# Kernel optimization log

Measured on AMD Instinct MI355X. Metric: run time of the kernel, lower is better.

## Reference

```python
import jax, jax.numpy as jnp
import numpy as np

EPS = 1e-12  # torch F.normalize eps

def _l2norm(v):
    return v / jnp.maximum(jnp.linalg.norm(v, axis=-1, keepdims=True), EPS)

def setup_inputs() -> dict:
    key = jax.random.key(0)
    x = jax.random.normal(key, (64, 64, 10, 512), dtype=jnp.float32)
    w = jnp.asarray(10.0, dtype=jnp.float32)
    b = jnp.asarray(-5.0, dtype=jnp.float32)
    return {"x": x, "w": w, "b": b}

def reference(x, w, b):
    B, N, M, D = x.shape
    NM = N * M
    x_flat = _l2norm(x.reshape(B, NM, D))                      # [B, NM, D]
    c_full = _l2norm(jnp.mean(x, axis=2))                      # [B, N, D]
    # leave-one-out centroid: (M * normalized_full_centroid - x) / (M - 1), then normalize
    c_excl = _l2norm(((M * c_full[:, :, None, :] - x) / (M - 1)).reshape(B, NM, D))  # [B, NM, D]
    # cosine sim of each utterance vs every (normalized) full centroid
    sim = jnp.einsum("bkd,bnd->bkn", x_flat, c_full)           # [B, NM, N]
    # replace own-speaker column with leave-one-out similarity (avoids [B,NM,N,D] blowup)
    excl_sim = jnp.sum(x_flat * c_excl, axis=-1)               # [B, NM]
    speaker_ids = jnp.repeat(jnp.arange(N), M)                 # [NM]
    rows = jnp.arange(NM)
    sim = sim.at[:, rows, speaker_ids].set(excl_sim)
    logits = w * sim + b                                       # [B, NM, N]
    logp = jax.nn.log_softmax(logits, axis=-1)
    # cross-entropy with targets = speaker_ids per row, mean over B*NM
    nll = -logp[:, rows, speaker_ids]                          # [B, NM]
    return jnp.mean(nll)
```

## Files before the change

kernel.cpp:

```cpp
#include <hip/hip_runtime.h>
#include <math.h>

static constexpr int Bn = 64;
static constexpr int Nn = 64;
static constexpr int Mn = 10;
static constexpr int Dn = 512;
static constexpr int NMn = Nn * Mn;
static constexpr int RT = 32;
static constexpr int NBLK2 = Bn * (NMn / RT);
static constexpr float EPSV = 1e-12f;

typedef unsigned short u16;
typedef unsigned int u32;
typedef __attribute__((ext_vector_type(8))) __bf16 bf16x8;
typedef __attribute__((ext_vector_type(4))) float f32x4;

static __device__ __forceinline__ u16 f2bf(float f) {
  u32 u = __float_as_uint(f);
  u = u + 0x7fffu + ((u >> 16) & 1u);
  return (u16)(u >> 16);
}


__global__ __launch_bounds__(256) void centroid_k(const float* __restrict__ x,
                                                  u16* __restrict__ ch2,
                                                  float* __restrict__ out) {
  const int bn = blockIdx.x;
  const int tid = threadIdx.x;
  const int f4 = tid & 127;
  const int mg = tid >> 7;
  const int wv = tid >> 6, ln = tid & 63;
  const float4* xp = (const float4*)(x + (size_t)bn * (Mn * Dn));

  if (bn == 0 && tid == 0) out[0] = 0.f;

  float4 a = {0.f, 0.f, 0.f, 0.f};
#pragma unroll
  for (int k = 0; k < 5; ++k) {
    const float4 v = xp[(2 * k + mg) * 128 + f4];
    a.x += v.x; a.y += v.y; a.z += v.z; a.w += v.w;
  }
  __shared__ float4 cred[128];
  if (mg == 1) cred[f4] = a;
  __syncthreads();

  float4 c = {0.f, 0.f, 0.f, 0.f};
  float cs = 0.f;
  if (mg == 0) {
    c = cred[f4];
    c.x += a.x; c.y += a.y; c.z += a.z; c.w += a.w;
    cs = c.x * c.x + c.y * c.y + c.z * c.z + c.w * c.w;
  }
#pragma unroll
  for (int t = 1; t < 64; t <<= 1) cs += __shfl_xor(cs, t, 64);
  __shared__ float csred[2];
  if (mg == 0 && ln == 0) csred[wv] = cs;
  __syncthreads();
  if (mg == 0) {
    const float scale = 1.0f / fmaxf(sqrtf(csred[0] + csred[1]), EPSV);
    const u16 h0 = f2bf(c.x * scale), h1 = f2bf(c.y * scale);
    const u16 h2 = f2bf(c.z * scale), h3 = f2bf(c.w * scale);
    uint2 w;
    w.x = (u32)h0 | ((u32)h1 << 16);
    w.y = (u32)h2 | ((u32)h3 << 16);
    const int n = bn & (Nn - 1), bb = bn >> 6;
    const size_t off = (((size_t)bb * 16 + (f4 >> 3)) * Nn + n) * 32 + ((f4 & 7) * 4);
    *(uint2*)(ch2 + off) = w;
  }
}

__global__ __launch_bounds__(512) void gemm_loss_k(const float* __restrict__ x,
                                                   const u16* __restrict__ ch2,
                                                   const float* __restrict__ wp,
                                                   const float* __restrict__ bp,
                                                   float* __restrict__ out) {
  __shared__ float S[8][16][65];
  __shared__ float SQ[2][4][16];
  __shared__ float nred[8];

  const int b = blockIdx.x / (NMn / RT);
  const int rt = blockIdx.x % (NMn / RT);
  const int row0 = rt * RT;
  const int tid = threadIdx.x, wv = tid >> 6, ln = tid & 63;
  const int lr = ln & 15;
  const int lkb = (ln >> 4) * 8;
  const int rh = wv >> 2;
  const int q = wv & 3;
  const int k0 = q * 128;

  const float* arow = x + ((size_t)b * NMn + row0 + rh * 16 + lr) * Dn + k0 + lkb;
  const u16* brow = ch2 + (((size_t)b * 16 + q * 4) * Nn) * 32 + (size_t)lr * 32 + lkb;

  f32x4 acc0 = {0.f, 0.f, 0.f, 0.f};
  f32x4 acc1 = acc0, acc2 = acc0, acc3 = acc0;
  float sq = 0.f;

#pragma unroll
  for (int kk = 0; kk < 128; kk += 32) {
    const u16* bp8 = brow + (size_t)(kk >> 5) * (Nn * 32);
    const float4 f0 = *(const float4*)(arow + kk);
    const float4 f1 = *(const float4*)(arow + kk + 4);
    const bf16x8 b0 = *(const bf16x8*)(bp8);
    const bf16x8 b1 = *(const bf16x8*)(bp8 + 16 * 32);
    const bf16x8 b2 = *(const bf16x8*)(bp8 + 32 * 32);
    const bf16x8 b3 = *(const bf16x8*)(bp8 + 48 * 32);
    const float v[8] = {f0.x, f0.y, f0.z, f0.w, f1.x, f1.y, f1.z, f1.w};
    bf16x8 ah;
#pragma unroll
    for (int i = 0; i < 8; ++i) {
      ah[i] = (__bf16)v[i];
      sq = fmaf(v[i], v[i], sq);
    }
    acc0 = __builtin_amdgcn_mfma_f32_16x16x32_bf16(ah, b0, acc0, 0, 0, 0);
    acc1 = __builtin_amdgcn_mfma_f32_16x16x32_bf16(ah, b1, acc1, 0, 0, 0);
    acc2 = __builtin_amdgcn_mfma_f32_16x16x32_bf16(ah, b2, acc2, 0, 0, 0);
    acc3 = __builtin_amdgcn_mfma_f32_16x16x32_bf16(ah, b3, acc3, 0, 0, 0);
  }

  sq += __shfl_xor(sq, 16, 64);
  sq += __shfl_xor(sq, 32, 64);
  if (ln < 16) SQ[rh][q][lr] = sq;

  const int orow = (ln >> 4) * 4;
#pragma unroll
  for (int r = 0; r < 4; ++r) {
    S[wv][orow + r][lr] = acc0[r];
    S[wv][orow + r][16 + lr] = acc1[r];
    S[wv][orow + r][32 + lr] = acc2[r];
    S[wv][orow + r][48 + lr] = acc3[r];
  }
  __syncthreads();

  const float W = *wp, Bb = *bp;
  float lane_nll = 0.f;
#pragma unroll
  for (int i = 0; i < 4; ++i) {
    const int R = wv * 4 + i;
    const int rhh = R >> 4, rl = R & 15;
    const int krow = row0 + R;
    const int spk = krow / Mn;
    const float rn = S[rhh * 4 + 0][rl][ln] + S[rhh * 4 + 1][rl][ln] +
                     S[rhh * 4 + 2][rl][ln] + S[rhh * 4 + 3][rl][ln];
    const float x2 = SQ[rhh][0][rl] + SQ[rhh][1][rl] + SQ[rhh][2][rl] + SQ[rhh][3][rl];
    const float xn = sqrtf(x2);
    const float inv_xn = 1.0f / fmaxf(xn, EPSV);
    float sv = rn * inv_xn;
    if (ln == spk) {
      const float num = (float)Mn * rn - x2;
      const float en = sqrtf(fmaxf((float)(Mn * Mn) - 2.0f * (float)Mn * rn + x2, 0.f));
      sv = num / fmaxf(xn * en, EPSV);
    }
    const float logit = W * sv + Bb;
    float e = expf(logit);
#pragma unroll
    for (int t = 1; t < 64; t <<= 1) e += __shfl_xor(e, t, 64);
    if (ln == 0) lane_nll += logf(e);
    if (ln == spk) lane_nll -= logit;
  }
#pragma unroll
  for (int t = 1; t < 64; t <<= 1) lane_nll += __shfl_xor(lane_nll, t, 64);
  if (ln == 0) nred[wv] = lane_nll;
  __syncthreads();
  if (tid == 0) {
    float s = 0.f;
#pragma unroll
    for (int i = 0; i < 8; ++i) s += nred[i];
    atomicAdd(out, s * (1.0f / (float)(Bn * NMn)));
  }
}

static constexpr int ROWS = 8;
static constexpr int DCHUNK = 128;
static constexpr int CPAD = DCHUNK + 1;

__global__ __launch_bounds__(256) void centroid_fb_k(const float* __restrict__ x,
                                                     float* __restrict__ c) {
  const int bn = blockIdx.x;
  const float* xp = x + (size_t)bn * Mn * Dn;
  const int tid = threadIdx.x;
  float a0 = 0.f, a1 = 0.f;
#pragma unroll
  for (int m = 0; m < Mn; ++m) {
    a0 += xp[m * Dn + tid];
    a1 += xp[m * Dn + tid + 256];
  }
  float s = a0 * a0 + a1 * a1;
#pragma unroll
  for (int m = 1; m < 64; m <<= 1) s += __shfl_xor(s, m, 64);
  __shared__ float red[4];
  const int wv = tid >> 6, ln = tid & 63;
  if (ln == 0) red[wv] = s;
  __syncthreads();
  const float tot = red[0] + red[1] + red[2] + red[3];
  const float scale = 1.0f / fmaxf(sqrtf(tot), EPSV);
  float* cp = c + (size_t)bn * Dn;
  cp[tid] = a0 * scale;
  cp[tid + 256] = a1 * scale;
}

__global__ __launch_bounds__(256) void loss_fb_k(const float* __restrict__ x,
                                                 const float* __restrict__ c,
                                                 const float* __restrict__ wp,
                                                 const float* __restrict__ bp,
                                                 float* __restrict__ out) {
  __shared__ __align__(16) float x_lds[ROWS * Dn];
  __shared__ float c_lds[Nn * CPAD];
  __shared__ float xn2s[ROWS];
  __shared__ float sim_lds[ROWS][Nn];

  const int tid = threadIdx.x;
  const int b = blockIdx.x / (NMn / ROWS);
  const int rblk = blockIdx.x % (NMn / ROWS);
  const int row0 = rblk * ROWS;
  const float* xrow = x + ((size_t)b * NMn + row0) * Dn;
  {
    const float4* xs = (const float4*)xrow;
    float4* xd = (float4*)x_lds;
#pragma unroll
    for (int i = tid; i < ROWS * Dn / 4; i += 256) xd[i] = xs[i];
  }
  __syncthreads();
  const int wv = tid >> 6, ln = tid & 63;
  for (int r = wv; r < ROWS; r += 4) {
    float s = 0.f;
#pragma unroll
    for (int j = ln; j < Dn; j += 64) {
      const float v = x_lds[r * Dn + j];
      s += v * v;
    }
#pragma unroll
    for (int m = 1; m < 64; m <<= 1) s += __shfl_xor(s, m, 64);
    if (ln == 0) xn2s[r] = s;
  }
  const int n = tid & 63;
  const int rg = tid >> 6;
  const int r0 = rg * 2, r1 = rg * 2 + 1;
  float s0 = 0.f, s1 = 0.f;
  const float* cb_base = c + (size_t)b * Nn * Dn;
  for (int cb = 0; cb < Dn; cb += DCHUNK) {
    __syncthreads();
    for (int i = tid; i < Nn * DCHUNK; i += 256) {
      const int nn = i / DCHUNK;
      const int j = i & (DCHUNK - 1);
      c_lds[nn * CPAD + j] = cb_base[(size_t)nn * Dn + cb + j];
    }
    __syncthreads();
#pragma unroll 16
    for (int j = 0; j < DCHUNK; ++j) {
      const float cv = c_lds[n * CPAD + j];
      s0 = fmaf(x_lds[r0 * Dn + cb + j], cv, s0);
      s1 = fmaf(x_lds[r1 * Dn + cb + j], cv, s1);
    }
  }
  sim_lds[r0][n] = s0;
  sim_lds[r1][n] = s1;
  __syncthreads();
  const float W = *wp, Bb = *bp;
  float acc_nll = 0.f;
  for (int r = wv; r < ROWS; r += 4) {
    const int k = row0 + r;
    const int spk = k / Mn;
    const float rn = sim_lds[r][ln];
    const float x2 = xn2s[r];
    const float xn = sqrtf(x2);
    const float inv_xn = 1.0f / fmaxf(xn, EPSV);
    const float rspk = sim_lds[r][spk];
    float sv = rn * inv_xn;
    if (ln == spk) {
      const float num = (float)Mn * rspk - x2;
      const float en = sqrtf(fmaxf((float)(Mn * Mn) - 2.0f * (float)Mn * rspk + x2, 0.f));
      sv = num / fmaxf(xn * en, EPSV);
    }
    const float logit = W * sv + Bb;
    const float lspk = __shfl(logit, spk, 64);
    float mx = logit;
#pragma unroll
    for (int m = 1; m < 64; m <<= 1) mx = fmaxf(mx, __shfl_xor(mx, m, 64));
    float se = expf(logit - mx);
#pragma unroll
    for (int m = 1; m < 64; m <<= 1) se += __shfl_xor(se, m, 64);
    acc_nll += (mx + logf(se)) - lspk;
  }
  __shared__ float nred[4];
  if (ln == 0) nred[wv] = acc_nll;
  __syncthreads();
  if (tid == 0)
    atomicAdd(out, (nred[0] + nred[1] + nred[2] + nred[3]) * (1.0f / (float)(Bn * NMn)));
}

extern "C" void kernel_launch(void* const* d_in, const int* in_sizes, int n_in,
                              void* d_out, int out_size, void* d_ws, size_t ws_size,
                              hipStream_t stream) {
  const float* x = (const float*)d_in[0];
  const float* w = (const float*)d_in[1];
  const float* b = (const float*)d_in[2];
  float* out = (float*)d_out;

  const size_t CSZ = (size_t)Bn * 16 * Nn * 32 * sizeof(u16);
  const size_t NEED = CSZ;

  if (ws_size >= NEED) {
    u16* ch2 = (u16*)d_ws;
    hipLaunchKernelGGL(centroid_k, dim3(Bn * Nn), dim3(256), 0, stream, x, ch2, out);
    hipLaunchKernelGGL(gemm_loss_k, dim3(NBLK2), dim3(512), 0, stream,
                       x, ch2, w, b, out);
  } else {
    float* c = (float*)d_ws;
    hipMemsetAsync(out, 0, sizeof(float), stream);
    hipLaunchKernelGGL(centroid_fb_k, dim3(Bn * Nn), dim3(256), 0, stream, x, c);
    hipLaunchKernelGGL(loss_fb_k, dim3(Bn * (NMn / ROWS)), dim3(256), 0, stream,
                       x, c, w, b, out);
  }
}
```

Baseline: 46.06 us.

## Process two speakers per centroid block and swizzle gemm block order across XCDs

The centroid kernel now handles two speakers per workgroup, which halves the grid and doubles the loads in flight per thread. The loss kernel remaps block IDs so that consecutive blocks on each of the 8 XCDs cover contiguous tiles of the same batch, aiming for better L2 locality of x and the centroid tiles. The trade-offs are higher register use and fewer blocks in the centroid kernel, and the swizzle assumes NBLK2 divides evenly by 8.

```diff
diff --git a/kernel.cpp b/kernel.cpp
--- a/kernel.cpp
+++ b/kernel.cpp
@@ -25,47 +25,63 @@
 __global__ __launch_bounds__(256) void centroid_k(const float* __restrict__ x,
                                                   u16* __restrict__ ch2,
                                                   float* __restrict__ out) {
-  const int bn = blockIdx.x;
+  const int base = blockIdx.x * 2;
   const int tid = threadIdx.x;
   const int f4 = tid & 127;
   const int mg = tid >> 7;
   const int wv = tid >> 6, ln = tid & 63;
-  const float4* xp = (const float4*)(x + (size_t)bn * (Mn * Dn));
-
-  if (bn == 0 && tid == 0) out[0] = 0.f;
-
-  float4 a = {0.f, 0.f, 0.f, 0.f};
+
+  if (blockIdx.x == 0 && tid == 0) out[0] = 0.f;
+
+  const float4* xp0 = (const float4*)(x + (size_t)base * (Mn * Dn));
+  const float4* xp1 = (const float4*)(x + (size_t)(base + 1) * (Mn * Dn));
+
+  float4 a0 = {0.f, 0.f, 0.f, 0.f}, a1 = {0.f, 0.f, 0.f, 0.f};
 #pragma unroll
   for (int k = 0; k < 5; ++k) {
-    const float4 v = xp[(2 * k + mg) * 128 + f4];
-    a.x += v.x; a.y += v.y; a.z += v.z; a.w += v.w;
-  }
-  __shared__ float4 cred[128];
-  if (mg == 1) cred[f4] = a;
-  __syncthreads();
-
-  float4 c = {0.f, 0.f, 0.f, 0.f};
-  float cs = 0.f;
+    const float4 v0 = xp0[(2 * k + mg) * 128 + f4];
+    const float4 v1 = xp1[(2 * k + mg) * 128 + f4];
+    a0.x += v0.x; a0.y += v0.y; a0.z += v0.z; a0.w += v0.w;
+    a1.x += v1.x; a1.y += v1.y; a1.z += v1.z; a1.w += v1.w;
+  }
+  __shared__ float4 cred[2][128];
+  if (mg == 1) { cred[0][f4] = a0; cred[1][f4] = a1; }
+  __syncthreads();
+
+  float cs0 = 0.f, cs1 = 0.f;
+  float4 c0 = {0.f, 0.f, 0.f, 0.f}, c1 = {0.f, 0.f, 0.f, 0.f};
   if (mg == 0) {
-    c = cred[f4];
-    c.x += a.x; c.y += a.y; c.z += a.z; c.w += a.w;
-    cs = c.x * c.x + c.y * c.y + c.z * c.z + c.w * c.w;
-  }
-#pragma unroll
-  for (int t = 1; t < 64; t <<= 1) cs += __shfl_xor(cs, t, 64);
-  __shared__ float csred[2];
-  if (mg == 0 && ln == 0) csred[wv] = cs;
+    const float4 v0 = cred[0][f4];
+    c0.x = a0.x + v0.x; c0.y = a0.y + v0.y; c0.z = a0.z + v0.z; c0.w = a0.w + v0.w;
+    cs0 = c0.x * c0.x + c0.y * c0.y + c0.z * c0.z + c0.w * c0.w;
+    const float4 v1 = cred[1][f4];
+    c1.x = a1.x + v1.x; c1.y = a1.y + v1.y; c1.z = a1.z + v1.z; c1.w = a1.w + v1.w;
+    cs1 = c1.x * c1.x + c1.y * c1.y + c1.z * c1.z + c1.w * c1.w;
+  }
+#pragma unroll
+  for (int t = 1; t < 64; t <<= 1) {
+    cs0 += __shfl_xor(cs0, t, 64);
+    cs1 += __shfl_xor(cs1, t, 64);
+  }
+  __shared__ float csred[2][2];
+  if (mg == 0 && ln == 0) { csred[0][wv] = cs0; csred[1][wv] = cs1; }
   __syncthreads();
   if (mg == 0) {
-    const float scale = 1.0f / fmaxf(sqrtf(csred[0] + csred[1]), EPSV);
-    const u16 h0 = f2bf(c.x * scale), h1 = f2bf(c.y * scale);
-    const u16 h2 = f2bf(c.z * scale), h3 = f2bf(c.w * scale);
-    uint2 w;
-    w.x = (u32)h0 | ((u32)h1 << 16);
-    w.y = (u32)h2 | ((u32)h3 << 16);
-    const int n = bn & (Nn - 1), bb = bn >> 6;
-    const size_t off = (((size_t)bb * 16 + (f4 >> 3)) * Nn + n) * 32 + ((f4 & 7) * 4);
-    *(uint2*)(ch2 + off) = w;
+    const int kblk = f4 >> 3, koff = (f4 & 7) * 4;
+#pragma unroll
+    for (int t = 0; t < 2; ++t) {
+      const int bn = base + t;
+      const int n = bn & (Nn - 1), bb = bn >> 6;
+      const float scale = 1.0f / fmaxf(sqrtf(csred[t][0] + csred[t][1]), EPSV);
+      const float4 c = t ? c1 : c0;
+      const u16 h0 = f2bf(c.x * scale), h1 = f2bf(c.y * scale);
+      const u16 h2 = f2bf(c.z * scale), h3 = f2bf(c.w * scale);
+      uint2 w;
+      w.x = (u32)h0 | ((u32)h1 << 16);
+      w.y = (u32)h2 | ((u32)h3 << 16);
+      const size_t off = (((size_t)bb * 16 + kblk) * Nn + n) * 32 + koff;
+      *(uint2*)(ch2 + off) = w;
+    }
   }
 }
 
@@ -78,8 +94,10 @@
   __shared__ float SQ[2][4][16];
   __shared__ float nred[8];
 
-  const int b = blockIdx.x / (NMn / RT);
-  const int rt = blockIdx.x % (NMn / RT);
+  const int bid = blockIdx.x;
+  const int wgid = (bid & 7) * (NBLK2 / 8) + (bid >> 3);
+  const int b = wgid / (NMn / RT);
+  const int rt = wgid % (NMn / RT);
   const int row0 = rt * RT;
   const int tid = threadIdx.x, wv = tid >> 6, ln = tid & 63;
   const int lr = ln & 15;
@@ -301,7 +319,8 @@
 
   if (ws_size >= NEED) {
     u16* ch2 = (u16*)d_ws;
-    hipLaunchKernelGGL(centroid_k, dim3(Bn * Nn), dim3(256), 0, stream, x, ch2, out);
+    hipLaunchKernelGGL(centroid_k, dim3(Bn * Nn / 2), dim3(256), 0, stream,
+                       x, ch2, out);
     hipLaunchKernelGGL(gemm_loss_k, dim3(NBLK2), dim3(512), 0, stream,
                        x, ch2, w, b, out);
   } else {
```

Result: no change. 45.80 us (-0.5%).
